# Kernel optimization log

Hardware: AMD Instinct MI355X
Metric: run time of the kernel (lower is better)

Reference implementation:

```python
import jax, jax.numpy as jnp
import numpy as np

B, S, D = 2, 2048, 1024
H, DH = 16, 64          # n_heads, d_head = d_model // n_heads
WINDOW = 128            # sliding-window size (causal, includes self)


def setup_inputs() -> dict:
    key = jax.random.key(0)
    k1, k2, k3 = jax.random.split(key, 3)
    x = jax.random.normal(k1, (B, S, D), dtype=jnp.float32)
    w_qkv = jax.random.normal(k2, (D, 3 * D), dtype=jnp.float32) * (1.0 / np.sqrt(D))
    w_out = jax.random.normal(k3, (D, D), dtype=jnp.float32) * (1.0 / np.sqrt(D))
    return {"x": x, "w_qkv": w_qkv, "w_out": w_out}


def reference(x, w_qkv, w_out):
    b, s, d = x.shape
    # QKV projection (no bias): [B,S,3D] -> [B,S,3,H,DH]
    qkv = (x @ w_qkv).reshape(b, s, 3, H, DH)
    q, k, v = qkv[:, :, 0], qkv[:, :, 1], qkv[:, :, 2]  # each [B,S,H,DH]
    scale = 1.0 / np.sqrt(DH)
    # Dense scores [B,H,S,S], as the explicit-mask SDPA path computes
    scores = jnp.einsum("bihd,bjhd->bhij", q, k) * scale
    i = jnp.arange(s)[:, None]
    j = jnp.arange(s)[None, :]
    # allowed: causal AND within sliding window of WINDOW positions (incl. self)
    allowed = (j <= i) & (j > i - WINDOW)
    scores = jnp.where(allowed, scores, -jnp.inf)
    attn = jax.nn.softmax(scores, axis=-1)
    out = jnp.einsum("bhij,bjhd->bihd", attn, v).reshape(b, s, d)
    return out @ w_out
```

## Files before the change

### kernel.cpp

```cpp
#include <hip/hip_runtime.h>

#define SQ      2048
#define NB      2
#define NH      16
#define DHD     64
#define WIN     128
#define DMODEL  1024
#define TRIPLE  3072

typedef __attribute__((ext_vector_type(8))) short  short8;
typedef __attribute__((ext_vector_type(4))) float  f32x4;

__device__ __forceinline__ unsigned short f2bf(float f) {
  unsigned u = __float_as_uint(f);
  u += 0x7fff + ((u >> 16) & 1);
  return (unsigned short)(u >> 16);
}

__device__ __forceinline__ void load_lds16(const void* g, void* l) {
  __builtin_amdgcn_global_load_lds(
      (const __attribute__((address_space(1))) unsigned int*)g,
      (__attribute__((address_space(3))) unsigned int*)l, 16, 0, 0);
}

__global__ void cast_bf16_kernel(const float* __restrict__ in,
                                 unsigned short* __restrict__ out, int n4) {
  int idx = blockIdx.x * blockDim.x + threadIdx.x;
  if (idx >= n4) return;
  f32x4 v = ((const f32x4*)in)[idx];
  ushort4 o;
  o.x = f2bf(v[0]); o.y = f2bf(v[1]); o.z = f2bf(v[2]); o.w = f2bf(v[3]);
  ((ushort4*)out)[idx] = o;
}

__global__ void transpose_cast_kernel(const float* __restrict__ in,
                                      unsigned short* __restrict__ out,
                                      int K, int N) {
  __shared__ float tile[32][33];
  int n0 = blockIdx.x * 32, k0 = blockIdx.y * 32;
  int tx = threadIdx.x, ty = threadIdx.y;
#pragma unroll
  for (int r = 0; r < 4; ++r)
    tile[ty + 8 * r][tx] = in[(size_t)(k0 + ty + 8 * r) * N + (n0 + tx)];
  __syncthreads();
#pragma unroll
  for (int r = 0; r < 4; ++r)
    out[(size_t)(n0 + ty + 8 * r) * K + (k0 + tx)] = f2bf(tile[tx][ty + 8 * r]);
}

template <bool BF16OUT>
__global__ __launch_bounds__(256) void gemm_bt_kernel(
    const unsigned short* __restrict__ A,
    const unsigned short* __restrict__ Bt,
    void* __restrict__ Cv,
    int M, int N, int K) {
  __shared__ short lsA[128 * 64];
  __shared__ short lsB[128 * 64];
  int tid  = threadIdx.x;
  int wave = tid >> 6, lane = tid & 63;
  int quad = lane >> 4, l16 = lane & 15;
  int wm = (wave >> 1) * 64, wn = (wave & 1) * 64;
  int m0 = blockIdx.x * 128, n0 = blockIdx.y * 128;

  f32x4 acc[4][4] = {};

  const short* Ag = (const short*)A;
  const short* Bg = (const short*)Bt;

  int row8 = lane >> 3;
  int gcol = ((lane & 7) ^ row8) * 8;

  int sw = (l16 & 7) * 8;

  for (int k0 = 0; k0 < K; k0 += 64) {
    const short* Ab = Ag + (size_t)(m0 + wave * 32) * K + k0;
    const short* Bb = Bg + (size_t)(n0 + wave * 32) * K + k0;
#pragma unroll
    for (int inst = 0; inst < 4; ++inst) {
      int r = inst * 8 + row8;
      load_lds16(Ab + (size_t)r * K + gcol, &lsA[(wave * 32 + inst * 8) * 64]);
      load_lds16(Bb + (size_t)r * K + gcol, &lsB[(wave * 32 + inst * 8) * 64]);
    }
    __syncthreads();
#pragma unroll
    for (int ks = 0; ks < 2; ++ks) {
      short8 af[4], bf[4];
#pragma unroll
      for (int t = 0; t < 4; ++t) {
        int coff = ((ks * 32 + quad * 8) ^ sw);
        af[t] = *(const short8*)(&lsA[(wm + t * 16 + l16) * 64 + coff]);
        bf[t] = *(const short8*)(&lsB[(wn + t * 16 + l16) * 64 + coff]);
      }
#pragma unroll
      for (int mt = 0; mt < 4; ++mt)
#pragma unroll
        for (int nt = 0; nt < 4; ++nt)
          acc[mt][nt] = __builtin_amdgcn_mfma_f32_16x16x32_bf16(
              af[mt], bf[nt], acc[mt][nt], 0, 0, 0);
    }
    __syncthreads();
  }
#pragma unroll
  for (int mt = 0; mt < 4; ++mt)
#pragma unroll
    for (int nt = 0; nt < 4; ++nt)
#pragma unroll
      for (int r = 0; r < 4; ++r) {
        int row = m0 + wm + mt * 16 + quad * 4 + r;
        int col = n0 + wn + nt * 16 + l16;
        if (BF16OUT)
          ((unsigned short*)Cv)[(size_t)row * N + col] = f2bf(acc[mt][nt][r]);
        else
          ((float*)Cv)[(size_t)row * N + col] = acc[mt][nt][r];
      }
}

#define KSTR 72
#define VSTR 40
#define PSTR 36
__global__ __launch_bounds__(256) void attn_kernel(
    const unsigned short* __restrict__ qkvb,
    unsigned short* __restrict__ attnout) {
  __shared__ short Kl[2][32 * KSTR];
  __shared__ short Vt[2][64 * VSTR];
  __shared__ short Pl[4][16 * PSTR];

  int i0 = blockIdx.x * 64, h = blockIdx.y, b = blockIdx.z;
  int tid = threadIdx.x, wave = tid >> 6, lane = tid & 63;
  int quad = lane >> 4, l16 = lane & 15;
  const unsigned short* base = qkvb + (size_t)b * SQ * TRIPLE;

  short8 qa[2];
  {
    int qi = i0 + wave * 16 + l16;
    const unsigned short* qrow = base + (size_t)qi * TRIPLE + h * DHD;
    qa[0] = *(const short8*)(qrow + quad * 8);
    qa[1] = *(const short8*)(qrow + 32 + quad * 8);
  }

  f32x4 o[4] = {};
  float mrow[4] = {-1e30f, -1e30f, -1e30f, -1e30f};
  float lrow[4] = {0.f, 0.f, 0.f, 0.f};

  int cstart = (i0 >= WIN) ? 0 : ((WIN - i0) >> 5);
  int nch = 6 - cstart;
  int jc0 = i0 - WIN + cstart * 32;

  int srow_ = tid >> 3;
  int scol_ = (tid & 7) * 8;

  auto stage = [&](int c, int bb) {
    int j = jc0 + c * 32 + srow_;
    const unsigned short* kr = base + (size_t)j * TRIPLE + DMODEL + h * DHD + scol_;
    *(short8*)(&Kl[bb][srow_ * KSTR + scol_]) = *(const short8*)kr;
    const unsigned short* vr = base + (size_t)j * TRIPLE + 2 * DMODEL + h * DHD + scol_;
    short8 vv = *(const short8*)vr;
#pragma unroll
    for (int e = 0; e < 8; ++e)
      Vt[bb][(scol_ + e) * VSTR + srow_] = vv[e];
  };

  stage(0, 0);
  __syncthreads();

  int irow = i0 + wave * 16 + quad * 4;

  for (int c = 0; c < nch; ++c) {
    int bb = c & 1;
    if (c + 1 < nch) stage(c + 1, bb ^ 1);
    int jc = jc0 + c * 32;

    f32x4 s[2] = {};
#pragma unroll
    for (int ks = 0; ks < 2; ++ks) {
#pragma unroll
      for (int nt = 0; nt < 2; ++nt) {
        short8 bk = *(const short8*)(&Kl[bb][(nt * 16 + l16) * KSTR + ks * 32 + quad * 8]);
        s[nt] = __builtin_amdgcn_mfma_f32_16x16x32_bf16(qa[ks], bk, s[nt], 0, 0, 0);
      }
    }
#pragma unroll
    for (int nt = 0; nt < 2; ++nt)
#pragma unroll
      for (int r = 0; r < 4; ++r) {
        int i_ = irow + r;
        int j_ = jc + nt * 16 + l16;
        bool ok = (j_ <= i_) && (j_ > i_ - WIN);
        s[nt][r] = ok ? s[nt][r] * 0.125f : -1e30f;
      }
    float rm[4];
#pragma unroll
    for (int r = 0; r < 4; ++r) rm[r] = fmaxf(s[0][r], s[1][r]);
#pragma unroll
    for (int off = 1; off < 16; off <<= 1)
#pragma unroll
      for (int r = 0; r < 4; ++r) rm[r] = fmaxf(rm[r], __shfl_xor(rm[r], off, 64));
    float al[4];
#pragma unroll
    for (int r = 0; r < 4; ++r) {
      float mn = fmaxf(mrow[r], rm[r]);
      al[r] = __expf(mrow[r] - mn);
      mrow[r] = mn;
    }
    f32x4 p[2];
#pragma unroll
    for (int nt = 0; nt < 2; ++nt)
#pragma unroll
      for (int r = 0; r < 4; ++r) p[nt][r] = __expf(s[nt][r] - mrow[r]);
    float rs[4];
#pragma unroll
    for (int r = 0; r < 4; ++r) rs[r] = p[0][r] + p[1][r];
#pragma unroll
    for (int off = 1; off < 16; off <<= 1)
#pragma unroll
      for (int r = 0; r < 4; ++r) rs[r] += __shfl_xor(rs[r], off, 64);
#pragma unroll
    for (int r = 0; r < 4; ++r) lrow[r] = lrow[r] * al[r] + rs[r];
#pragma unroll
    for (int nt = 0; nt < 4; ++nt)
#pragma unroll
      for (int r = 0; r < 4; ++r) o[nt][r] *= al[r];
#pragma unroll
    for (int nt = 0; nt < 2; ++nt)
#pragma unroll
      for (int r = 0; r < 4; ++r)
        Pl[wave][(quad * 4 + r) * PSTR + nt * 16 + l16] = f2bf(p[nt][r]);
    short8 pa = *(const short8*)(&Pl[wave][l16 * PSTR + quad * 8]);
#pragma unroll
    for (int nt = 0; nt < 4; ++nt) {
      short8 bv = *(const short8*)(&Vt[bb][(nt * 16 + l16) * VSTR + quad * 8]);
      o[nt] = __builtin_amdgcn_mfma_f32_16x16x32_bf16(pa, bv, o[nt], 0, 0, 0);
    }
    __syncthreads();
  }

  float inv[4];
#pragma unroll
  for (int r = 0; r < 4; ++r) inv[r] = 1.0f / lrow[r];
#pragma unroll
  for (int nt = 0; nt < 4; ++nt)
#pragma unroll
    for (int r = 0; r < 4; ++r) {
      int i_ = irow + r;
      int d_ = nt * 16 + l16;
      attnout[(size_t)(b * SQ + i_) * DMODEL + h * DHD + d_] = f2bf(o[nt][r] * inv[r]);
    }
}

extern "C" void kernel_launch(void* const* d_in, const int* in_sizes, int n_in,
                              void* d_out, int out_size, void* d_ws, size_t ws_size,
                              hipStream_t stream) {
  const float* x     = (const float*)d_in[0];
  const float* w_qkv = (const float*)d_in[1];
  const float* w_out = (const float*)d_in[2];
  float* out = (float*)d_out;

  char* ws = (char*)d_ws;
  unsigned short* xb    = (unsigned short*)(ws);
  unsigned short* wqkvT = (unsigned short*)(ws + 8388608);
  unsigned short* woutT = (unsigned short*)(ws + 14680064);
  unsigned short* qkvb  = (unsigned short*)(ws + 16777216);
  unsigned short* attn  = (unsigned short*)(ws + 41943040);

  cast_bf16_kernel<<<4096, 256, 0, stream>>>(x, xb, (NB * SQ * DMODEL) / 4);
  dim3 tb(32, 8);
  transpose_cast_kernel<<<dim3(TRIPLE / 32, DMODEL / 32), tb, 0, stream>>>(w_qkv, wqkvT, DMODEL, TRIPLE);
  transpose_cast_kernel<<<dim3(DMODEL / 32, DMODEL / 32), tb, 0, stream>>>(w_out, woutT, DMODEL, DMODEL);
  gemm_bt_kernel<true><<<dim3((NB * SQ) / 128, TRIPLE / 128), 256, 0, stream>>>(
      xb, wqkvT, qkvb, NB * SQ, TRIPLE, DMODEL);
  attn_kernel<<<dim3(SQ / 64, NH, NB), 256, 0, stream>>>(qkvb, attn);
  gemm_bt_kernel<false><<<dim3((NB * SQ) / 128, DMODEL / 128), 256, 0, stream>>>(
      attn, woutT, out, NB * SQ, DMODEL, DMODEL);
}
```

Baseline: 160.2 us.

## Fuse prep casts into one kernel and stage full KV window in attention

Merges the x cast and the two weight transpose-casts into a single prep kernel launch, dispatching on block index. The attention kernel now loads the whole 192-row K/V window into shared memory up front and processes 64-key chunks without per-chunk barriers or double buffering. This removes two launches and the per-chunk synchronisation, and widens the MFMA work per chunk. In exchange it uses more LDS, which may lower occupancy, and it no longer overlaps K/V loading with compute.

```diff
diff --git a/kernel.cpp b/kernel.cpp
--- a/kernel.cpp
+++ b/kernel.cpp
@@ -23,22 +23,29 @@
       (__attribute__((address_space(3))) unsigned int*)l, 16, 0, 0);
 }
 
-__global__ void cast_bf16_kernel(const float* __restrict__ in,
-                                 unsigned short* __restrict__ out, int n4) {
-  int idx = blockIdx.x * blockDim.x + threadIdx.x;
-  if (idx >= n4) return;
-  f32x4 v = ((const f32x4*)in)[idx];
-  ushort4 o;
-  o.x = f2bf(v[0]); o.y = f2bf(v[1]); o.z = f2bf(v[2]); o.w = f2bf(v[3]);
-  ((ushort4*)out)[idx] = o;
-}
-
-__global__ void transpose_cast_kernel(const float* __restrict__ in,
-                                      unsigned short* __restrict__ out,
-                                      int K, int N) {
+__global__ __launch_bounds__(256) void prep_kernel(
+    const float* __restrict__ x, const float* __restrict__ w_qkv,
+    const float* __restrict__ w_out,
+    unsigned short* __restrict__ xb, unsigned short* __restrict__ wqkvT,
+    unsigned short* __restrict__ woutT) {
   __shared__ float tile[32][33];
-  int n0 = blockIdx.x * 32, k0 = blockIdx.y * 32;
-  int tx = threadIdx.x, ty = threadIdx.y;
+  int blk = blockIdx.x, tid = threadIdx.x;
+  if (blk < 4096) {
+    int idx = blk * 256 + tid;
+    f32x4 v = ((const f32x4*)x)[idx];
+    ushort4 o;
+    o.x = f2bf(v[0]); o.y = f2bf(v[1]); o.z = f2bf(v[2]); o.w = f2bf(v[3]);
+    ((ushort4*)xb)[idx] = o;
+    return;
+  }
+  const float* in;
+  unsigned short* out;
+  int K = DMODEL, N, t;
+  if (blk < 7168) { in = w_qkv; out = wqkvT; N = TRIPLE;  t = blk - 4096; }
+  else            { in = w_out; out = woutT; N = DMODEL;  t = blk - 7168; }
+  int ntiles = N / 32;
+  int n0 = (t % ntiles) * 32, k0 = (t / ntiles) * 32;
+  int tx = tid & 31, ty = tid >> 5;
 #pragma unroll
   for (int r = 0; r < 4; ++r)
     tile[ty + 8 * r][tx] = in[(size_t)(k0 + ty + 8 * r) * N + (n0 + tx)];
@@ -69,7 +76,6 @@
 
   int row8 = lane >> 3;
   int gcol = ((lane & 7) ^ row8) * 8;
-
   int sw = (l16 & 7) * 8;
 
   for (int k0 = 0; k0 < K; k0 += 64) {
@@ -116,13 +122,13 @@
 }
 
 #define KSTR 72
-#define VSTR 40
-#define PSTR 36
+#define VSTR 200
+#define PSTR 72
 __global__ __launch_bounds__(256) void attn_kernel(
     const unsigned short* __restrict__ qkvb,
     unsigned short* __restrict__ attnout) {
-  __shared__ short Kl[2][32 * KSTR];
-  __shared__ short Vt[2][64 * VSTR];
+  __shared__ short Kl[192 * KSTR];
+  __shared__ short Vt[64 * VSTR];
   __shared__ short Pl[4][16 * PSTR];
 
   int i0 = blockIdx.x * 64, h = blockIdx.y, b = blockIdx.z;
@@ -138,49 +144,42 @@
     qa[1] = *(const short8*)(qrow + 32 + quad * 8);
   }
 
+  int jbase = (i0 >= WIN) ? (i0 - WIN) : 0;
+  int nch = (i0 + 64 - jbase) >> 6;
+
+  int srow_ = tid >> 3;
+  int scol_ = (tid & 7) * 8;
+  for (int p = 0; p < 2 * nch; ++p) {
+    int r = p * 32 + srow_;
+    int j = jbase + r;
+    const unsigned short* kr = base + (size_t)j * TRIPLE + DMODEL + h * DHD + scol_;
+    *(short8*)(&Kl[r * KSTR + scol_]) = *(const short8*)kr;
+    const unsigned short* vr = base + (size_t)j * TRIPLE + 2 * DMODEL + h * DHD + scol_;
+    short8 vv = *(const short8*)vr;
+#pragma unroll
+    for (int e = 0; e < 8; ++e)
+      Vt[(scol_ + e) * VSTR + r] = vv[e];
+  }
+  __syncthreads();
+
   f32x4 o[4] = {};
   float mrow[4] = {-1e30f, -1e30f, -1e30f, -1e30f};
   float lrow[4] = {0.f, 0.f, 0.f, 0.f};
-
-  int cstart = (i0 >= WIN) ? 0 : ((WIN - i0) >> 5);
-  int nch = 6 - cstart;
-  int jc0 = i0 - WIN + cstart * 32;
-
-  int srow_ = tid >> 3;
-  int scol_ = (tid & 7) * 8;
-
-  auto stage = [&](int c, int bb) {
-    int j = jc0 + c * 32 + srow_;
-    const unsigned short* kr = base + (size_t)j * TRIPLE + DMODEL + h * DHD + scol_;
-    *(short8*)(&Kl[bb][srow_ * KSTR + scol_]) = *(const short8*)kr;
-    const unsigned short* vr = base + (size_t)j * TRIPLE + 2 * DMODEL + h * DHD + scol_;
-    short8 vv = *(const short8*)vr;
-#pragma unroll
-    for (int e = 0; e < 8; ++e)
-      Vt[bb][(scol_ + e) * VSTR + srow_] = vv[e];
-  };
-
-  stage(0, 0);
-  __syncthreads();
-
   int irow = i0 + wave * 16 + quad * 4;
 
   for (int c = 0; c < nch; ++c) {
-    int bb = c & 1;
-    if (c + 1 < nch) stage(c + 1, bb ^ 1);
-    int jc = jc0 + c * 32;
-
-    f32x4 s[2] = {};
-#pragma unroll
-    for (int ks = 0; ks < 2; ++ks) {
-#pragma unroll
-      for (int nt = 0; nt < 2; ++nt) {
-        short8 bk = *(const short8*)(&Kl[bb][(nt * 16 + l16) * KSTR + ks * 32 + quad * 8]);
+    int jc = jbase + c * 64;
+
+    f32x4 s[4] = {};
+#pragma unroll
+    for (int ks = 0; ks < 2; ++ks)
+#pragma unroll
+      for (int nt = 0; nt < 4; ++nt) {
+        short8 bk = *(const short8*)(&Kl[(c * 64 + nt * 16 + l16) * KSTR + ks * 32 + quad * 8]);
         s[nt] = __builtin_amdgcn_mfma_f32_16x16x32_bf16(qa[ks], bk, s[nt], 0, 0, 0);
       }
-    }
-#pragma unroll
-    for (int nt = 0; nt < 2; ++nt)
+#pragma unroll
+    for (int nt = 0; nt < 4; ++nt)
 #pragma unroll
       for (int r = 0; r < 4; ++r) {
         int i_ = irow + r;
@@ -190,7 +189,8 @@
       }
     float rm[4];
 #pragma unroll
-    for (int r = 0; r < 4; ++r) rm[r] = fmaxf(s[0][r], s[1][r]);
+    for (int r = 0; r < 4; ++r)
+      rm[r] = fmaxf(fmaxf(s[0][r], s[1][r]), fmaxf(s[2][r], s[3][r]));
 #pragma unroll
     for (int off = 1; off < 16; off <<= 1)
 #pragma unroll
@@ -202,14 +202,15 @@
       al[r] = __expf(mrow[r] - mn);
       mrow[r] = mn;
     }
-    f32x4 p[2];
-#pragma unroll
-    for (int nt = 0; nt < 2; ++nt)
+    f32x4 p[4];
+#pragma unroll
+    for (int nt = 0; nt < 4; ++nt)
 #pragma unroll
       for (int r = 0; r < 4; ++r) p[nt][r] = __expf(s[nt][r] - mrow[r]);
     float rs[4];
 #pragma unroll
-    for (int r = 0; r < 4; ++r) rs[r] = p[0][r] + p[1][r];
+    for (int r = 0; r < 4; ++r)
+      rs[r] = (p[0][r] + p[1][r]) + (p[2][r] + p[3][r]);
 #pragma unroll
     for (int off = 1; off < 16; off <<= 1)
 #pragma unroll
@@ -221,17 +222,20 @@
 #pragma unroll
       for (int r = 0; r < 4; ++r) o[nt][r] *= al[r];
 #pragma unroll
-    for (int nt = 0; nt < 2; ++nt)
+    for (int nt = 0; nt < 4; ++nt)
 #pragma unroll
       for (int r = 0; r < 4; ++r)
         Pl[wave][(quad * 4 + r) * PSTR + nt * 16 + l16] = f2bf(p[nt][r]);
-    short8 pa = *(const short8*)(&Pl[wave][l16 * PSTR + quad * 8]);
-#pragma unroll
-    for (int nt = 0; nt < 4; ++nt) {
-      short8 bv = *(const short8*)(&Vt[bb][(nt * 16 + l16) * VSTR + quad * 8]);
-      o[nt] = __builtin_amdgcn_mfma_f32_16x16x32_bf16(pa, bv, o[nt], 0, 0, 0);
-    }
-    __syncthreads();
+    short8 pa[2];
+    pa[0] = *(const short8*)(&Pl[wave][l16 * PSTR + quad * 8]);
+    pa[1] = *(const short8*)(&Pl[wave][l16 * PSTR + 32 + quad * 8]);
+#pragma unroll
+    for (int ks = 0; ks < 2; ++ks)
+#pragma unroll
+      for (int nt = 0; nt < 4; ++nt) {
+        short8 bv = *(const short8*)(&Vt[(nt * 16 + l16) * VSTR + c * 64 + ks * 32 + quad * 8]);
+        o[nt] = __builtin_amdgcn_mfma_f32_16x16x32_bf16(pa[ks], bv, o[nt], 0, 0, 0);
+      }
   }
 
   float inv[4];
@@ -262,10 +266,7 @@
   unsigned short* qkvb  = (unsigned short*)(ws + 16777216);
   unsigned short* attn  = (unsigned short*)(ws + 41943040);
 
-  cast_bf16_kernel<<<4096, 256, 0, stream>>>(x, xb, (NB * SQ * DMODEL) / 4);
-  dim3 tb(32, 8);
-  transpose_cast_kernel<<<dim3(TRIPLE / 32, DMODEL / 32), tb, 0, stream>>>(w_qkv, wqkvT, DMODEL, TRIPLE);
-  transpose_cast_kernel<<<dim3(DMODEL / 32, DMODEL / 32), tb, 0, stream>>>(w_out, woutT, DMODEL, DMODEL);
+  prep_kernel<<<8192, 256, 0, stream>>>(x, w_qkv, w_out, xb, wqkvT, woutT);
   gemm_bt_kernel<true><<<dim3((NB * SQ) / 128, TRIPLE / 128), 256, 0, stream>>>(
       xb, wqkvT, qkvb, NB * SQ, TRIPLE, DMODEL);
   attn_kernel<<<dim3(SQ / 64, NH, NB), 256, 0, stream>>>(qkvb, attn);
```

Result: faster. 153.6 us (-4.1%).
